# Kernel tuning notes

Hardware: AMD Instinct MI355X
Metric: run time of the kernel (lower is better)

## Reference

```python
import jax, jax.numpy as jnp
import numpy as np

INTENT_DIM = 64
HIDDEN_DIM = 128
B = 16384
M = 32


def setup_inputs() -> dict:
    key = jax.random.key(0)
    ks = jax.random.split(key, 12)
    d_in = INTENT_DIM + 4
    s = lambda n: 1.0 / np.sqrt(n)
    return {
        "ego_z": jax.random.normal(ks[0], (B, INTENT_DIM), jnp.float32),
        "neighbor_zs": jax.random.normal(ks[1], (B, M, INTENT_DIM), jnp.float32),
        "neighbor_rel_pos": jax.random.normal(ks[2], (B, M, 4), jnp.float32),
        "mask": jax.random.randint(ks[3], (B, M), 0, 2, jnp.int32),
        "Wq": jax.random.uniform(ks[4], (INTENT_DIM, HIDDEN_DIM), jnp.float32, -s(INTENT_DIM), s(INTENT_DIM)),
        "bq": jnp.zeros((HIDDEN_DIM,), jnp.float32),
        "Wk": jax.random.uniform(ks[5], (d_in, HIDDEN_DIM), jnp.float32, -s(d_in), s(d_in)),
        "bk": jnp.zeros((HIDDEN_DIM,), jnp.float32),
        "Wv": jax.random.uniform(ks[6], (d_in, HIDDEN_DIM), jnp.float32, -s(d_in), s(d_in)),
        "bv": jnp.zeros((HIDDEN_DIM,), jnp.float32),
        "Wo": jax.random.uniform(ks[7], (HIDDEN_DIM, INTENT_DIM), jnp.float32, -s(HIDDEN_DIM), s(HIDDEN_DIM)),
        "bo": jnp.zeros((INTENT_DIM,), jnp.float32),
    }


def reference(ego_z, neighbor_zs, neighbor_rel_pos, mask,
              Wq, bq, Wk, bk, Wv, bv, Wo, bo):
    # concat neighbor intent + relative position: (B, M, intent+4)
    feats = jnp.concatenate([neighbor_zs, neighbor_rel_pos], axis=-1)
    q = ego_z @ Wq + bq                       # (B, H)
    k = feats @ Wk + bk                       # (B, M, H)
    v = feats @ Wv + bv                       # (B, M, H)
    scores = jnp.einsum("bh,bmh->bm", q, k) / jnp.sqrt(jnp.float32(HIDDEN_DIM))
    scores = jnp.where(mask == 0, jnp.float32(-1e9), scores)
    weights = jax.nn.softmax(scores, axis=-1)  # (B, M)
    ctx = jnp.einsum("bm,bmh->bh", weights, v)  # (B, H)
    return ctx @ Wo + bo                        # (B, intent)
```

## Files before the change

kernel.cpp:

```cpp
#include <hip/hip_runtime.h>
#include <math.h>

#define M       32
#define IDIM    64
#define DIN     68
#define HDIM    128

#define WS_A4     0
#define WS_WVO4   4352
#define WS_U0     8704
#define WS_G      8772
#define WS_C0     8836
#define WS_OUTB   8840
#define WS_FLOATS 8904

#define CST_FLOATS 8704
#define CST_WVO    4352

template <int CTRL>
__device__ __forceinline__ float dpp_add(float x) {
  int t = __builtin_amdgcn_update_dpp(0, __float_as_int(x), CTRL, 0xF, 0xF, true);
  return x + __int_as_float(t);
}
__device__ __forceinline__ float red4(float x) {
  x = dpp_add<0xB1>(x);
  x = dpp_add<0x4E>(x);
  return x;
}
__device__ __forceinline__ float red16(float x) {
  x = dpp_add<0xB1>(x);
  x = dpp_add<0x4E>(x);
  x = dpp_add<0x124>(x);
  x = dpp_add<0x128>(x);
  return x;
}

#define SEG_A   0
#define SEG_W   17408
#define SEG_U0  34816
#define SEG_G   35088
#define SEG_OB  35344
#define SEG_C0  35600
#define PRE_T   35601

__global__ __launch_bounds__(256)
void ga_precompute(const float* __restrict__ Wq, const float* __restrict__ bq,
                   const float* __restrict__ Wk, const float* __restrict__ bk,
                   const float* __restrict__ Wv, const float* __restrict__ bv,
                   const float* __restrict__ Wo, const float* __restrict__ bo,
                   float* __restrict__ ws) {
  int t = blockIdx.x * 256 + threadIdx.x;
  if (t >= PRE_T) return;
  const float4* Wq4 = (const float4*)Wq;
  const float4* Wk4 = (const float4*)Wk;
  const float4* Wv4 = (const float4*)Wv;
  const float4* bq4 = (const float4*)bq;
  const float4* bk4 = (const float4*)bk;
  const int sub = t & 3;
  const int h4b = sub * 8;

  if (t < SEG_W) {
    int e = t >> 2;
    int k = e & 3, rem = e >> 2;
    int d = rem % DIN, i4 = rem / DIN;
    int i = i4 * 4 + k;
    float acc = 0.f;
    #pragma unroll
    for (int hh = 0; hh < 8; ++hh) {
      float4 a = Wq4[i*32 + h4b + hh], b = Wk4[d*32 + h4b + hh];
      acc = fmaf(a.x, b.x, acc); acc = fmaf(a.y, b.y, acc);
      acc = fmaf(a.z, b.z, acc); acc = fmaf(a.w, b.w, acc);
    }
    acc = red4(acc);
    if (sub == 0) ws[WS_A4 + e] = acc;
  } else if (t < SEG_U0) {
    int e = (t - SEG_W) >> 2;
    int k = e & 3, rem = e >> 2;
    int j = rem & 63, d4 = rem >> 6;
    int d = d4 * 4 + k;
    float acc = 0.f;
    #pragma unroll
    for (int hh = 0; hh < 8; ++hh) {
      float4 v = Wv4[d*32 + h4b + hh];
      int h = (h4b + hh) * 4;
      acc = fmaf(v.x, Wo[(h    )*IDIM + j], acc);
      acc = fmaf(v.y, Wo[(h + 1)*IDIM + j], acc);
      acc = fmaf(v.z, Wo[(h + 2)*IDIM + j], acc);
      acc = fmaf(v.w, Wo[(h + 3)*IDIM + j], acc);
    }
    acc = red4(acc);
    if (sub == 0) ws[WS_WVO4 + e] = acc;
  } else if (t < SEG_G) {
    int d = (t - SEG_U0) >> 2;
    float acc = 0.f;
    #pragma unroll
    for (int hh = 0; hh < 8; ++hh) {
      float4 a = Wk4[d*32 + h4b + hh], b = bq4[h4b + hh];
      acc = fmaf(a.x, b.x, acc); acc = fmaf(a.y, b.y, acc);
      acc = fmaf(a.z, b.z, acc); acc = fmaf(a.w, b.w, acc);
    }
    acc = red4(acc);
    if (sub == 0) ws[WS_U0 + d] = acc;
  } else if (t < SEG_OB) {
    int i = (t - SEG_G) >> 2;
    float acc = 0.f;
    #pragma unroll
    for (int hh = 0; hh < 8; ++hh) {
      float4 a = Wq4[i*32 + h4b + hh], b = bk4[h4b + hh];
      acc = fmaf(a.x, b.x, acc); acc = fmaf(a.y, b.y, acc);
      acc = fmaf(a.z, b.z, acc); acc = fmaf(a.w, b.w, acc);
    }
    acc = red4(acc);
    if (sub == 0) ws[WS_G + i] = acc;
  } else if (t < SEG_C0) {
    int j = (t - SEG_OB) >> 2;
    float acc = 0.f;
    #pragma unroll
    for (int hh = 0; hh < 8; ++hh) {
      int h = (h4b + hh) * 4;
      acc = fmaf(bv[h    ], Wo[(h    )*IDIM + j], acc);
      acc = fmaf(bv[h + 1], Wo[(h + 1)*IDIM + j], acc);
      acc = fmaf(bv[h + 2], Wo[(h + 2)*IDIM + j], acc);
      acc = fmaf(bv[h + 3], Wo[(h + 3)*IDIM + j], acc);
    }
    acc = red4(acc);
    if (sub == 0) ws[WS_OUTB + j] = acc + bo[j];
  } else {
    float acc = 0.f;
    for (int h = 0; h < HDIM; ++h) acc = fmaf(bq[h], bk[h], acc);
    ws[WS_C0] = acc;
  }
}

__global__ __launch_bounds__(512, 4)
void ga_main(const float* __restrict__ ego,
             const float* __restrict__ nz,
             const float* __restrict__ rp,
             const int*   __restrict__ mask,
             const float* __restrict__ ws,
             float* __restrict__ out) {
  __shared__ float cst   [CST_FLOATS];
  __shared__ float u_lds [8 * 64];
  __shared__ float fb_lds[8 * 64];

  const int tid  = threadIdx.x;
  const int wave = tid >> 6;
  const int lane = tid & 63;
  const int t4   = lane >> 4;
  const int l    = lane & 15;
  const int row  = __builtin_amdgcn_readfirstlane(blockIdx.x * 8 + wave);

  #define GLL(K) do { int c = wave + 8*(K); if (c < 34)                         \
    __builtin_amdgcn_global_load_lds(                                           \
      (const __attribute__((address_space(1))) void*)(ws + c*256 + lane*4),     \
      (__attribute__((address_space(3))) void*)(cst + c*256), 16, 0, 0); } while(0)
  GLL(0); GLL(1); GLL(2); GLL(3); GLL(4);
  #undef GLL
  __builtin_amdgcn_sched_barrier(0);

  const float4* zsrc4 = (const float4*)(nz + (size_t)row * (M * IDIM));
  float4 z0 = zsrc4[0*64 + lane], z1 = zsrc4[1*64 + lane];
  float4 z2 = zsrc4[2*64 + lane], z3 = zsrc4[3*64 + lane];
  float4 z4 = zsrc4[4*64 + lane], z5 = zsrc4[5*64 + lane];
  float4 z6 = zsrc4[6*64 + lane], z7 = zsrc4[7*64 + lane];
  const float4* rpsrc = (const float4*)(rp + (size_t)row * (M * 4));
  const float4 rpa = rpsrc[4 * (lane & 7) + t4];
  const int    mreg = mask[row * M + (lane & 31)];

  __builtin_amdgcn_sched_barrier(0);
  asm volatile("s_waitcnt vmcnt(10)" ::: "memory");
  __builtin_amdgcn_s_barrier();
  asm volatile("" ::: "memory");

  const float* egoR = ego + (size_t)row * IDIM;
  {
    float ua0 = 0.f, ua1 = 0.f, ua2 = 0.f, ua3 = 0.f;
    #pragma unroll 8
    for (int i4 = 0; i4 < 16; ++i4) {
      const float4 av = *(const float4*)&cst[(i4 * DIN + lane) << 2];
      ua0 = fmaf(egoR[i4 * 4],     av.x, ua0);
      ua1 = fmaf(egoR[i4 * 4 + 1], av.y, ua1);
      ua2 = fmaf(egoR[i4 * 4 + 2], av.z, ua2);
      ua3 = fmaf(egoR[i4 * 4 + 3], av.w, ua3);
    }
    u_lds[wave * 64 + lane] = ((ua0 + ua1) + (ua2 + ua3)) + ws[WS_U0 + lane];
  }
  float rpdot;
  {
    const float4 av = *(const float4*)&cst[(l * DIN + IDIM + t4) << 2];
    float pt = egoR[l * 4] * av.x;
    pt = fmaf(egoR[l * 4 + 1], av.y, pt);
    pt = fmaf(egoR[l * 4 + 2], av.z, pt);
    pt = fmaf(egoR[l * 4 + 3], av.w, pt);
    pt = red16(pt);
    int pti = __float_as_int(pt);
    float uh0 = __int_as_float(__builtin_amdgcn_readlane(pti, 0))  + ws[WS_U0 + 64];
    float uh1 = __int_as_float(__builtin_amdgcn_readlane(pti, 16)) + ws[WS_U0 + 65];
    float uh2 = __int_as_float(__builtin_amdgcn_readlane(pti, 32)) + ws[WS_U0 + 66];
    float uh3 = __int_as_float(__builtin_amdgcn_readlane(pti, 48)) + ws[WS_U0 + 67];
    rpdot = fmaf(rpa.w, uh3, fmaf(rpa.z, uh2, fmaf(rpa.y, uh1, rpa.x * uh0)));
  }
  float cterm;
  {
    float pc = egoR[lane] * ws[WS_G + lane];
    pc = red16(pc);
    pc += __shfl_xor(pc, 16);
    pc += __shfl_xor(pc, 32);
    cterm = pc + ws[WS_C0];
  }

  asm volatile("" ::: "memory");

  const float4 u4 = *(const float4*)&u_lds[wave * 64 + l * 4];
  const unsigned int mbits  = (unsigned int)__ballot(mreg != 0);
  const unsigned int mshift = mbits >> t4;

  #define SC(IT, Z) float s##IT; {                                        \
    float p = (Z).x * u4.x;                                               \
    p = fmaf((Z).y, u4.y, p);                                             \
    p = fmaf((Z).z, u4.z, p);                                             \
    p = fmaf((Z).w, u4.w, p);                                             \
    p += (l == (IT)) ? rpdot : 0.f;                                       \
    p = red16(p);                                                         \
    s##IT = ((mshift >> (4*(IT))) & 1u)                                   \
          ? (p + cterm) * 0.088388347648318447f : -1e9f; }
  SC(0, z0) SC(1, z1) SC(2, z2) SC(3, z3)
  SC(4, z4) SC(5, z5) SC(6, z6) SC(7, z7)
  #undef SC

  float mx = fmaxf(fmaxf(fmaxf(s0, s1), fmaxf(s2, s3)),
                   fmaxf(fmaxf(s4, s5), fmaxf(s6, s7)));
  mx = fmaxf(mx, __shfl_xor(mx, 16));
  mx = fmaxf(mx, __shfl_xor(mx, 32));
  float e0 = __expf(s0 - mx), e1 = __expf(s1 - mx);
  float e2 = __expf(s2 - mx), e3 = __expf(s3 - mx);
  float e4 = __expf(s4 - mx), e5 = __expf(s5 - mx);
  float e6 = __expf(s6 - mx), e7 = __expf(s7 - mx);
  float se = ((e0 + e1) + (e2 + e3)) + ((e4 + e5) + (e6 + e7));
  se += __shfl_xor(se, 16);
  se += __shfl_xor(se, 32);
  const float rse = __builtin_amdgcn_rcpf(se);
  const float w0 = e0 * rse, w1 = e1 * rse, w2 = e2 * rse, w3 = e3 * rse;
  const float w4 = e4 * rse, w5 = e5 * rse, w6 = e6 * rse, w7 = e7 * rse;

  float p40 = 0.f, p41 = 0.f, p42 = 0.f, p43 = 0.f;
  #define FB(W, Z) do {                                                   \
    p40 = fmaf((W), (Z).x, p40);                                          \
    p41 = fmaf((W), (Z).y, p41);                                          \
    p42 = fmaf((W), (Z).z, p42);                                          \
    p43 = fmaf((W), (Z).w, p43);                                          \
  } while (0);
  FB(w0, z0) FB(w1, z1) FB(w2, z2) FB(w3, z3)
  FB(w4, z4) FB(w5, z5) FB(w6, z6) FB(w7, z7)
  #undef FB
  p40 += __shfl_xor(p40, 16);  p40 += __shfl_xor(p40, 32);
  p41 += __shfl_xor(p41, 16);  p41 += __shfl_xor(p41, 32);
  p42 += __shfl_xor(p42, 16);  p42 += __shfl_xor(p42, 32);
  p43 += __shfl_xor(p43, 16);  p43 += __shfl_xor(p43, 32);
  if (lane < 16) {
    float4 fv; fv.x = p40; fv.y = p41; fv.z = p42; fv.w = p43;
    *(float4*)&fb_lds[wave * 64 + l * 4] = fv;
  }

  float wsel;
  {
    float a0 = (l & 1) ? w1 : w0, a1 = (l & 1) ? w3 : w2;
    float a2 = (l & 1) ? w5 : w4, a3 = (l & 1) ? w7 : w6;
    float b0 = (l & 2) ? a1 : a0, b1 = (l & 2) ? a3 : a2;
    wsel = 0.5f * ((l & 4) ? b1 : b0);
  }
  float pr0 = wsel * rpa.x, pr1 = wsel * rpa.y;
  float pr2 = wsel * rpa.z, pr3 = wsel * rpa.w;
  pr0 = red16(pr0); pr0 += __shfl_xor(pr0, 16); pr0 += __shfl_xor(pr0, 32);
  pr1 = red16(pr1); pr1 += __shfl_xor(pr1, 16); pr1 += __shfl_xor(pr1, 32);
  pr2 = red16(pr2); pr2 += __shfl_xor(pr2, 16); pr2 += __shfl_xor(pr2, 32);
  pr3 = red16(pr3); pr3 += __shfl_xor(pr3, 16); pr3 += __shfl_xor(pr3, 32);

  asm volatile("" ::: "memory");

  float oa0 = 0.f, oa1 = 0.f, oa2 = 0.f, oa3 = 0.f;
  #pragma unroll 8
  for (int d4 = 0; d4 < 16; ++d4) {
    const float4 wv = *(const float4*)&cst[CST_WVO + ((d4 * IDIM + lane) << 2)];
    const float4 fv = *(const float4*)&fb_lds[wave * 64 + d4 * 4];
    oa0 = fmaf(fv.x, wv.x, oa0);
    oa1 = fmaf(fv.y, wv.y, oa1);
    oa2 = fmaf(fv.z, wv.z, oa2);
    oa3 = fmaf(fv.w, wv.w, oa3);
  }
  {
    const float4 wv = *(const float4*)&cst[CST_WVO + ((16 * IDIM + lane) << 2)];
    oa0 = fmaf(pr0, wv.x, oa0);
    oa1 = fmaf(pr1, wv.y, oa1);
    oa2 = fmaf(pr2, wv.z, oa2);
    oa3 = fmaf(pr3, wv.w, oa3);
  }
  out[(size_t)row * IDIM + lane] = ((oa0 + oa1) + (oa2 + oa3)) + ws[WS_OUTB + lane];
}

extern "C" void kernel_launch(void* const* d_in, const int* in_sizes, int n_in,
                              void* d_out, int out_size, void* d_ws, size_t ws_size,
                              hipStream_t stream) {
  const float* ego = (const float*)d_in[0];
  const float* nz  = (const float*)d_in[1];
  const float* rp  = (const float*)d_in[2];
  const int*   mk  = (const int*)d_in[3];
  const float* Wq  = (const float*)d_in[4];
  const float* bq  = (const float*)d_in[5];
  const float* Wk  = (const float*)d_in[6];
  const float* bk  = (const float*)d_in[7];
  const float* Wv  = (const float*)d_in[8];
  const float* bv  = (const float*)d_in[9];
  const float* Wo  = (const float*)d_in[10];
  const float* bo  = (const float*)d_in[11];
  float* ws = (float*)d_ws;
  float* o  = (float*)d_out;

  const int nrows = in_sizes[0] / IDIM;

  ga_precompute<<<(PRE_T + 255) / 256, 256, 0, stream>>>(
      Wq, bq, Wk, bk, Wv, bv, Wo, bo, ws);
  ga_main<<<nrows / 8, 512, 0, stream>>>(ego, nz, rp, mk, ws, o);
}
```

Measured before the change: 38.24 us.

## Process two rows per wave with software-prefetch of next row's neighbors

Each wave now handles two batch rows instead of one, halving the grid. While the first row's softmax-weighted sum is finishing, the second row's neighbor features, relative positions and mask are loaded into registers, so the global load latency overlaps compute. The per-block constant LDS fill is also amortized over twice as many rows. The cost is higher register pressure, fewer blocks to hide latency, and a reuse of the ego-row and rpa registers that must stay consistent with the prefetch.

```diff
diff --git a/kernel.cpp b/kernel.cpp
--- a/kernel.cpp
+++ b/kernel.cpp
@@ -148,7 +148,20 @@
   const int lane = tid & 63;
   const int t4   = lane >> 4;
   const int l    = lane & 15;
-  const int row  = __builtin_amdgcn_readfirstlane(blockIdx.x * 8 + wave);
+  const int row0 = blockIdx.x * 16 + wave;
+
+  float4 z0, z1, z2, z3, z4, z5, z6, z7, rpa;
+  int mreg;
+
+  #define LOADROW(R) do {                                                      \
+    const float4* zs = (const float4*)(nz + (size_t)(R) * (M * IDIM));         \
+    z0 = zs[0*64 + lane]; z1 = zs[1*64 + lane];                                \
+    z2 = zs[2*64 + lane]; z3 = zs[3*64 + lane];                                \
+    z4 = zs[4*64 + lane]; z5 = zs[5*64 + lane];                                \
+    z6 = zs[6*64 + lane]; z7 = zs[7*64 + lane];                                \
+    rpa  = ((const float4*)(rp + (size_t)(R) * (M * 4)))[4 * (lane & 7) + t4]; \
+    mreg = mask[(R) * M + (lane & 31)];                                        \
+  } while (0)
 
   #define GLL(K) do { int c = wave + 8*(K); if (c < 34)                         \
     __builtin_amdgcn_global_load_lds(                                           \
@@ -158,144 +171,159 @@
   #undef GLL
   __builtin_amdgcn_sched_barrier(0);
 
-  const float4* zsrc4 = (const float4*)(nz + (size_t)row * (M * IDIM));
-  float4 z0 = zsrc4[0*64 + lane], z1 = zsrc4[1*64 + lane];
-  float4 z2 = zsrc4[2*64 + lane], z3 = zsrc4[3*64 + lane];
-  float4 z4 = zsrc4[4*64 + lane], z5 = zsrc4[5*64 + lane];
-  float4 z6 = zsrc4[6*64 + lane], z7 = zsrc4[7*64 + lane];
-  const float4* rpsrc = (const float4*)(rp + (size_t)row * (M * 4));
-  const float4 rpa = rpsrc[4 * (lane & 7) + t4];
-  const int    mreg = mask[row * M + (lane & 31)];
-
+  LOADROW(row0);
   __builtin_amdgcn_sched_barrier(0);
   asm volatile("s_waitcnt vmcnt(10)" ::: "memory");
   __builtin_amdgcn_s_barrier();
   asm volatile("" ::: "memory");
 
-  const float* egoR = ego + (size_t)row * IDIM;
+  #define PROCESS(R, NR) do {                                                  \
+    const int rr = __builtin_amdgcn_readfirstlane(R);                          \
+    const float* egoR = ego + (size_t)rr * IDIM;                               \
+                                                            \
+    {                                                                          \
+      float ua0 = 0.f, ua1 = 0.f, ua2 = 0.f, ua3 = 0.f;                        \
+      _Pragma("unroll 8")                                                      \
+      for (int i4 = 0; i4 < 16; ++i4) {                                        \
+        const float4 av = *(const float4*)&cst[(i4 * DIN + lane) << 2];        \
+        ua0 = fmaf(egoR[i4 * 4],     av.x, ua0);                               \
+        ua1 = fmaf(egoR[i4 * 4 + 1], av.y, ua1);                               \
+        ua2 = fmaf(egoR[i4 * 4 + 2], av.z, ua2);                               \
+        ua3 = fmaf(egoR[i4 * 4 + 3], av.w, ua3);                               \
+      }                                                                        \
+      u_lds[wave * 64 + lane] = ((ua0 + ua1) + (ua2 + ua3)) + ws[WS_U0 + lane];\
+    }                                                                          \
+    float rpdot;                                                               \
+    {                                                                          \
+      const float4 av = *(const float4*)&cst[(l * DIN + IDIM + t4) << 2];      \
+      float pt = egoR[l * 4] * av.x;                                           \
+      pt = fmaf(egoR[l * 4 + 1], av.y, pt);                                    \
+      pt = fmaf(egoR[l * 4 + 2], av.z, pt);                                    \
+      pt = fmaf(egoR[l * 4 + 3], av.w, pt);                                    \
+      pt = red16(pt);                                                          \
+      int pti = __float_as_int(pt);                                            \
+      float uh0 = __int_as_float(__builtin_amdgcn_readlane(pti, 0))            \
+                + ws[WS_U0 + 64];                                              \
+      float uh1 = __int_as_float(__builtin_amdgcn_readlane(pti, 16))           \
+                + ws[WS_U0 + 65];                                              \
+      float uh2 = __int_as_float(__builtin_amdgcn_readlane(pti, 32))           \
+                + ws[WS_U0 + 66];                                              \
+      float uh3 = __int_as_float(__builtin_amdgcn_readlane(pti, 48))           \
+                + ws[WS_U0 + 67];                                              \
+      rpdot = fmaf(rpa.w, uh3, fmaf(rpa.z, uh2, fmaf(rpa.y, uh1,               \
+              rpa.x * uh0)));                                                  \
+    }                                                                          \
+    float cterm;                                                               \
+    {                                                                          \
+      float pc = egoR[lane] * ws[WS_G + lane];                                 \
+      pc = red16(pc);                                                          \
+      pc += __shfl_xor(pc, 16);                                                \
+      pc += __shfl_xor(pc, 32);                                                \
+      cterm = pc + ws[WS_C0];                                                  \
+    }                                                                          \
+    asm volatile("" ::: "memory");                                             \
+                                                          \
+    const float4 u4 = *(const float4*)&u_lds[wave * 64 + l * 4];               \
+    const unsigned int mbits  = (unsigned int)__ballot(mreg != 0);             \
+    const unsigned int mshift = mbits >> t4;                                   \
+    float s0, s1, s2, s3, s4, s5, s6, s7;                                      \
+    SC(0, z0, s0) SC(1, z1, s1) SC(2, z2, s2) SC(3, z3, s3)                    \
+    SC(4, z4, s4) SC(5, z5, s5) SC(6, z6, s6) SC(7, z7, s7)                    \
+    float mx = fmaxf(fmaxf(fmaxf(s0, s1), fmaxf(s2, s3)),                      \
+                     fmaxf(fmaxf(s4, s5), fmaxf(s6, s7)));                     \
+    mx = fmaxf(mx, __shfl_xor(mx, 16));                                        \
+    mx = fmaxf(mx, __shfl_xor(mx, 32));                                        \
+    float e0 = __expf(s0 - mx), e1 = __expf(s1 - mx);                          \
+    float e2 = __expf(s2 - mx), e3 = __expf(s3 - mx);                          \
+    float e4 = __expf(s4 - mx), e5 = __expf(s5 - mx);                          \
+    float e6 = __expf(s6 - mx), e7 = __expf(s7 - mx);                          \
+    float se = ((e0 + e1) + (e2 + e3)) + ((e4 + e5) + (e6 + e7));              \
+    se += __shfl_xor(se, 16);                                                  \
+    se += __shfl_xor(se, 32);                                                  \
+    const float rse = __builtin_amdgcn_rcpf(se);                               \
+    const float w0 = e0 * rse, w1 = e1 * rse, w2 = e2 * rse, w3 = e3 * rse;    \
+    const float w4 = e4 * rse, w5 = e5 * rse, w6 = e6 * rse, w7 = e7 * rse;    \
+                                                            \
+    float p40 = 0.f, p41 = 0.f, p42 = 0.f, p43 = 0.f;                          \
+    FBm(w0, z0) FBm(w1, z1) FBm(w2, z2) FBm(w3, z3)                            \
+    FBm(w4, z4) FBm(w5, z5) FBm(w6, z6) FBm(w7, z7)                            \
+     \
+    if ((NR) >= 0) { LOADROW(NR); }                                            \
+    p40 += __shfl_xor(p40, 16);  p40 += __shfl_xor(p40, 32);                   \
+    p41 += __shfl_xor(p41, 16);  p41 += __shfl_xor(p41, 32);                   \
+    p42 += __shfl_xor(p42, 16);  p42 += __shfl_xor(p42, 32);                   \
+    p43 += __shfl_xor(p43, 16);  p43 += __shfl_xor(p43, 32);                   \
+    if (lane < 16) {                                                           \
+      float4 fv; fv.x = p40; fv.y = p41; fv.z = p42; fv.w = p43;               \
+      *(float4*)&fb_lds[wave * 64 + l * 4] = fv;                               \
+    }                                                                          \
+                 \
+    float wsel;                                                                \
+    {                                                                          \
+      float a0 = (l & 1) ? w1 : w0, a1 = (l & 1) ? w3 : w2;                    \
+      float a2 = (l & 1) ? w5 : w4, a3 = (l & 1) ? w7 : w6;                    \
+      float b0 = (l & 2) ? a1 : a0, b1 = (l & 2) ? a3 : a2;                    \
+      wsel = 0.5f * ((l & 4) ? b1 : b0);                                       \
+    }                                                                          \
+    float pr0 = wsel * rpold.x, pr1 = wsel * rpold.y;                          \
+    float pr2 = wsel * rpold.z, pr3 = wsel * rpold.w;                          \
+    pr0 = red16(pr0); pr0 += __shfl_xor(pr0, 16); pr0 += __shfl_xor(pr0, 32);  \
+    pr1 = red16(pr1); pr1 += __shfl_xor(pr1, 16); pr1 += __shfl_xor(pr1, 32);  \
+    pr2 = red16(pr2); pr2 += __shfl_xor(pr2, 16); pr2 += __shfl_xor(pr2, 32);  \
+    pr3 = red16(pr3); pr3 += __shfl_xor(pr3, 16); pr3 += __shfl_xor(pr3, 32);  \
+    asm volatile("" ::: "memory");                                             \
+                                                                  \
+    float oa0 = 0.f, oa1 = 0.f, oa2 = 0.f, oa3 = 0.f;                          \
+    _Pragma("unroll 8")                                                        \
+    for (int d4 = 0; d4 < 16; ++d4) {                                          \
+      const float4 wv = *(const float4*)&cst[CST_WVO + ((d4*IDIM + lane)<<2)]; \
+      const float4 fv = *(const float4*)&fb_lds[wave * 64 + d4 * 4];           \
+      oa0 = fmaf(fv.x, wv.x, oa0);                                             \
+      oa1 = fmaf(fv.y, wv.y, oa1);                                             \
+      oa2 = fmaf(fv.z, wv.z, oa2);                                             \
+      oa3 = fmaf(fv.w, wv.w, oa3);                                             \
+    }                                                                          \
+    {                                                                          \
+      const float4 wv = *(const float4*)&cst[CST_WVO + ((16*IDIM + lane)<<2)]; \
+      oa0 = fmaf(pr0, wv.x, oa0);                                              \
+      oa1 = fmaf(pr1, wv.y, oa1);                                              \
+      oa2 = fmaf(pr2, wv.z, oa2);                                              \
+      oa3 = fmaf(pr3, wv.w, oa3);                                              \
+    }                                                                          \
+    out[(size_t)rr * IDIM + lane] =                                            \
+        ((oa0 + oa1) + (oa2 + oa3)) + ws[WS_OUTB + lane];                      \
+    asm volatile("" ::: "memory");                                             \
+  } while (0)
+
+  #define SC(IT, Z, SD) {                                                      \
+    float p = (Z).x * u4.x;                                                    \
+    p = fmaf((Z).y, u4.y, p);                                                  \
+    p = fmaf((Z).z, u4.z, p);                                                  \
+    p = fmaf((Z).w, u4.w, p);                                                  \
+    p += (l == (IT)) ? rpdot : 0.f;                                            \
+    p = red16(p);                                                              \
+    SD = ((mshift >> (4*(IT))) & 1u)                                           \
+       ? (p + cterm) * 0.088388347648318447f : -1e9f; }
+  #define FBm(W, Z) do {                                                       \
+    p40 = fmaf((W), (Z).x, p40);                                               \
+    p41 = fmaf((W), (Z).y, p41);                                               \
+    p42 = fmaf((W), (Z).z, p42);                                               \
+    p43 = fmaf((W), (Z).w, p43);                                               \
+  } while (0);
+
   {
-    float ua0 = 0.f, ua1 = 0.f, ua2 = 0.f, ua3 = 0.f;
-    #pragma unroll 8
-    for (int i4 = 0; i4 < 16; ++i4) {
-      const float4 av = *(const float4*)&cst[(i4 * DIN + lane) << 2];
-      ua0 = fmaf(egoR[i4 * 4],     av.x, ua0);
-      ua1 = fmaf(egoR[i4 * 4 + 1], av.y, ua1);
-      ua2 = fmaf(egoR[i4 * 4 + 2], av.z, ua2);
-      ua3 = fmaf(egoR[i4 * 4 + 3], av.w, ua3);
-    }
-    u_lds[wave * 64 + lane] = ((ua0 + ua1) + (ua2 + ua3)) + ws[WS_U0 + lane];
-  }
-  float rpdot;
-  {
-    const float4 av = *(const float4*)&cst[(l * DIN + IDIM + t4) << 2];
-    float pt = egoR[l * 4] * av.x;
-    pt = fmaf(egoR[l * 4 + 1], av.y, pt);
-    pt = fmaf(egoR[l * 4 + 2], av.z, pt);
-    pt = fmaf(egoR[l * 4 + 3], av.w, pt);
-    pt = red16(pt);
-    int pti = __float_as_int(pt);
-    float uh0 = __int_as_float(__builtin_amdgcn_readlane(pti, 0))  + ws[WS_U0 + 64];
-    float uh1 = __int_as_float(__builtin_amdgcn_readlane(pti, 16)) + ws[WS_U0 + 65];
-    float uh2 = __int_as_float(__builtin_amdgcn_readlane(pti, 32)) + ws[WS_U0 + 66];
-    float uh3 = __int_as_float(__builtin_amdgcn_readlane(pti, 48)) + ws[WS_U0 + 67];
-    rpdot = fmaf(rpa.w, uh3, fmaf(rpa.z, uh2, fmaf(rpa.y, uh1, rpa.x * uh0)));
-  }
-  float cterm;
-  {
-    float pc = egoR[lane] * ws[WS_G + lane];
-    pc = red16(pc);
-    pc += __shfl_xor(pc, 16);
-    pc += __shfl_xor(pc, 32);
-    cterm = pc + ws[WS_C0];
-  }
-
-  asm volatile("" ::: "memory");
-
-  const float4 u4 = *(const float4*)&u_lds[wave * 64 + l * 4];
-  const unsigned int mbits  = (unsigned int)__ballot(mreg != 0);
-  const unsigned int mshift = mbits >> t4;
-
-  #define SC(IT, Z) float s##IT; {                                        \
-    float p = (Z).x * u4.x;                                               \
-    p = fmaf((Z).y, u4.y, p);                                             \
-    p = fmaf((Z).z, u4.z, p);                                             \
-    p = fmaf((Z).w, u4.w, p);                                             \
-    p += (l == (IT)) ? rpdot : 0.f;                                       \
-    p = red16(p);                                                         \
-    s##IT = ((mshift >> (4*(IT))) & 1u)                                   \
-          ? (p + cterm) * 0.088388347648318447f : -1e9f; }
-  SC(0, z0) SC(1, z1) SC(2, z2) SC(3, z3)
-  SC(4, z4) SC(5, z5) SC(6, z6) SC(7, z7)
-  #undef SC
-
-  float mx = fmaxf(fmaxf(fmaxf(s0, s1), fmaxf(s2, s3)),
-                   fmaxf(fmaxf(s4, s5), fmaxf(s6, s7)));
-  mx = fmaxf(mx, __shfl_xor(mx, 16));
-  mx = fmaxf(mx, __shfl_xor(mx, 32));
-  float e0 = __expf(s0 - mx), e1 = __expf(s1 - mx);
-  float e2 = __expf(s2 - mx), e3 = __expf(s3 - mx);
-  float e4 = __expf(s4 - mx), e5 = __expf(s5 - mx);
-  float e6 = __expf(s6 - mx), e7 = __expf(s7 - mx);
-  float se = ((e0 + e1) + (e2 + e3)) + ((e4 + e5) + (e6 + e7));
-  se += __shfl_xor(se, 16);
-  se += __shfl_xor(se, 32);
-  const float rse = __builtin_amdgcn_rcpf(se);
-  const float w0 = e0 * rse, w1 = e1 * rse, w2 = e2 * rse, w3 = e3 * rse;
-  const float w4 = e4 * rse, w5 = e5 * rse, w6 = e6 * rse, w7 = e7 * rse;
-
-  float p40 = 0.f, p41 = 0.f, p42 = 0.f, p43 = 0.f;
-  #define FB(W, Z) do {                                                   \
-    p40 = fmaf((W), (Z).x, p40);                                          \
-    p41 = fmaf((W), (Z).y, p41);                                          \
-    p42 = fmaf((W), (Z).z, p42);                                          \
-    p43 = fmaf((W), (Z).w, p43);                                          \
-  } while (0);
-  FB(w0, z0) FB(w1, z1) FB(w2, z2) FB(w3, z3)
-  FB(w4, z4) FB(w5, z5) FB(w6, z6) FB(w7, z7)
-  #undef FB
-  p40 += __shfl_xor(p40, 16);  p40 += __shfl_xor(p40, 32);
-  p41 += __shfl_xor(p41, 16);  p41 += __shfl_xor(p41, 32);
-  p42 += __shfl_xor(p42, 16);  p42 += __shfl_xor(p42, 32);
-  p43 += __shfl_xor(p43, 16);  p43 += __shfl_xor(p43, 32);
-  if (lane < 16) {
-    float4 fv; fv.x = p40; fv.y = p41; fv.z = p42; fv.w = p43;
-    *(float4*)&fb_lds[wave * 64 + l * 4] = fv;
-  }
-
-  float wsel;
-  {
-    float a0 = (l & 1) ? w1 : w0, a1 = (l & 1) ? w3 : w2;
-    float a2 = (l & 1) ? w5 : w4, a3 = (l & 1) ? w7 : w6;
-    float b0 = (l & 2) ? a1 : a0, b1 = (l & 2) ? a3 : a2;
-    wsel = 0.5f * ((l & 4) ? b1 : b0);
-  }
-  float pr0 = wsel * rpa.x, pr1 = wsel * rpa.y;
-  float pr2 = wsel * rpa.z, pr3 = wsel * rpa.w;
-  pr0 = red16(pr0); pr0 += __shfl_xor(pr0, 16); pr0 += __shfl_xor(pr0, 32);
-  pr1 = red16(pr1); pr1 += __shfl_xor(pr1, 16); pr1 += __shfl_xor(pr1, 32);
-  pr2 = red16(pr2); pr2 += __shfl_xor(pr2, 16); pr2 += __shfl_xor(pr2, 32);
-  pr3 = red16(pr3); pr3 += __shfl_xor(pr3, 16); pr3 += __shfl_xor(pr3, 32);
-
-  asm volatile("" ::: "memory");
-
-  float oa0 = 0.f, oa1 = 0.f, oa2 = 0.f, oa3 = 0.f;
-  #pragma unroll 8
-  for (int d4 = 0; d4 < 16; ++d4) {
-    const float4 wv = *(const float4*)&cst[CST_WVO + ((d4 * IDIM + lane) << 2)];
-    const float4 fv = *(const float4*)&fb_lds[wave * 64 + d4 * 4];
-    oa0 = fmaf(fv.x, wv.x, oa0);
-    oa1 = fmaf(fv.y, wv.y, oa1);
-    oa2 = fmaf(fv.z, wv.z, oa2);
-    oa3 = fmaf(fv.w, wv.w, oa3);
+    const float4 rpold = rpa;
+    PROCESS(row0, row0 + 8);
   }
   {
-    const float4 wv = *(const float4*)&cst[CST_WVO + ((16 * IDIM + lane) << 2)];
-    oa0 = fmaf(pr0, wv.x, oa0);
-    oa1 = fmaf(pr1, wv.y, oa1);
-    oa2 = fmaf(pr2, wv.z, oa2);
-    oa3 = fmaf(pr3, wv.w, oa3);
+    const float4 rpold = rpa;
+    PROCESS(row0 + 8, -1);
   }
-  out[(size_t)row * IDIM + lane] = ((oa0 + oa1) + (oa2 + oa3)) + ws[WS_OUTB + lane];
+
+  #undef PROCESS
+  #undef SC
+  #undef FBm
+  #undef LOADROW
 }
 
 extern "C" void kernel_launch(void* const* d_in, const int* in_sizes, int n_in,
@@ -320,5 +348,5 @@
 
   ga_precompute<<<(PRE_T + 255) / 256, 256, 0, stream>>>(
       Wq, bq, Wk, bk, Wv, bv, Wo, bo, ws);
-  ga_main<<<nrows / 8, 512, 0, stream>>>(ego, nz, rp, mk, ws, o);
-}
+  ga_main<<<nrows / 16, 512, 0, stream>>>(ego, nz, rp, mk, ws, o);
+}
```

After: 38.49 us. No clear change (+0.7%).

## Read fused Wv·Wo weights from global/L2 and broadcast fb via readlane

Applied to the files above, without the earlier changes.

Stops staging the second weight block (WvWo) into LDS, which halves the shared-memory footprint and the global_load_lds preamble. The final projection now reads those weights directly from global memory, where they should be L2-cached. The per-row fb vector is broadcast with v_readlane instead of a round trip through LDS. This should allow higher occupancy and shorter block startup, at the cost of global-load latency inside the output loop and sixty-four scalar readlanes.

```diff
diff --git a/kernel.cpp b/kernel.cpp
--- a/kernel.cpp
+++ b/kernel.cpp
@@ -14,8 +14,7 @@
 #define WS_OUTB   8840
 #define WS_FLOATS 8904
 
-#define CST_FLOATS 8704
-#define CST_WVO    4352
+#define CST_FLOATS 4352
 
 template <int CTRL>
 __device__ __forceinline__ float dpp_add(float x) {
@@ -33,6 +32,9 @@
   x = dpp_add<0x124>(x);
   x = dpp_add<0x128>(x);
   return x;
+}
+__device__ __forceinline__ float rdlane(float x, int sl) {
+  return __int_as_float(__builtin_amdgcn_readlane(__float_as_int(x), sl));
 }
 
 #define SEG_A   0
@@ -139,9 +141,8 @@
              const int*   __restrict__ mask,
              const float* __restrict__ ws,
              float* __restrict__ out) {
-  __shared__ float cst   [CST_FLOATS];
-  __shared__ float u_lds [8 * 64];
-  __shared__ float fb_lds[8 * 64];
+  __shared__ float cst  [CST_FLOATS];
+  __shared__ float u_lds[8 * 64];
 
   const int tid  = threadIdx.x;
   const int wave = tid >> 6;
@@ -150,11 +151,11 @@
   const int l    = lane & 15;
   const int row  = __builtin_amdgcn_readfirstlane(blockIdx.x * 8 + wave);
 
-  #define GLL(K) do { int c = wave + 8*(K); if (c < 34)                         \
+  #define GLL(K) do { int c = wave + 8*(K); if (c < 17)                         \
     __builtin_amdgcn_global_load_lds(                                           \
       (const __attribute__((address_space(1))) void*)(ws + c*256 + lane*4),     \
       (__attribute__((address_space(3))) void*)(cst + c*256), 16, 0, 0); } while(0)
-  GLL(0); GLL(1); GLL(2); GLL(3); GLL(4);
+  GLL(0); GLL(1); GLL(2);
   #undef GLL
   __builtin_amdgcn_sched_barrier(0);
 
@@ -193,11 +194,10 @@
     pt = fmaf(egoR[l * 4 + 2], av.z, pt);
     pt = fmaf(egoR[l * 4 + 3], av.w, pt);
     pt = red16(pt);
-    int pti = __float_as_int(pt);
-    float uh0 = __int_as_float(__builtin_amdgcn_readlane(pti, 0))  + ws[WS_U0 + 64];
-    float uh1 = __int_as_float(__builtin_amdgcn_readlane(pti, 16)) + ws[WS_U0 + 65];
-    float uh2 = __int_as_float(__builtin_amdgcn_readlane(pti, 32)) + ws[WS_U0 + 66];
-    float uh3 = __int_as_float(__builtin_amdgcn_readlane(pti, 48)) + ws[WS_U0 + 67];
+    float uh0 = rdlane(pt, 0)  + ws[WS_U0 + 64];
+    float uh1 = rdlane(pt, 16) + ws[WS_U0 + 65];
+    float uh2 = rdlane(pt, 32) + ws[WS_U0 + 66];
+    float uh3 = rdlane(pt, 48) + ws[WS_U0 + 67];
     rpdot = fmaf(rpa.w, uh3, fmaf(rpa.z, uh2, fmaf(rpa.y, uh1, rpa.x * uh0)));
   }
   float cterm;
@@ -257,10 +257,6 @@
   p41 += __shfl_xor(p41, 16);  p41 += __shfl_xor(p41, 32);
   p42 += __shfl_xor(p42, 16);  p42 += __shfl_xor(p42, 32);
   p43 += __shfl_xor(p43, 16);  p43 += __shfl_xor(p43, 32);
-  if (lane < 16) {
-    float4 fv; fv.x = p40; fv.y = p41; fv.z = p42; fv.w = p43;
-    *(float4*)&fb_lds[wave * 64 + l * 4] = fv;
-  }
 
   float wsel;
   {
@@ -276,20 +272,18 @@
   pr2 = red16(pr2); pr2 += __shfl_xor(pr2, 16); pr2 += __shfl_xor(pr2, 32);
   pr3 = red16(pr3); pr3 += __shfl_xor(pr3, 16); pr3 += __shfl_xor(pr3, 32);
 
-  asm volatile("" ::: "memory");
-
+  const float4* wvo4 = (const float4*)(ws + WS_WVO4);
   float oa0 = 0.f, oa1 = 0.f, oa2 = 0.f, oa3 = 0.f;
-  #pragma unroll 8
+  #pragma unroll
   for (int d4 = 0; d4 < 16; ++d4) {
-    const float4 wv = *(const float4*)&cst[CST_WVO + ((d4 * IDIM + lane) << 2)];
-    const float4 fv = *(const float4*)&fb_lds[wave * 64 + d4 * 4];
-    oa0 = fmaf(fv.x, wv.x, oa0);
-    oa1 = fmaf(fv.y, wv.y, oa1);
-    oa2 = fmaf(fv.z, wv.z, oa2);
-    oa3 = fmaf(fv.w, wv.w, oa3);
-  }
-  {
-    const float4 wv = *(const float4*)&cst[CST_WVO + ((16 * IDIM + lane) << 2)];
+    const float4 wv = wvo4[d4 * IDIM + lane];
+    oa0 = fmaf(rdlane(p40, d4), wv.x, oa0);
+    oa1 = fmaf(rdlane(p41, d4), wv.y, oa1);
+    oa2 = fmaf(rdlane(p42, d4), wv.z, oa2);
+    oa3 = fmaf(rdlane(p43, d4), wv.w, oa3);
+  }
+  {
+    const float4 wv = wvo4[16 * IDIM + lane];
     oa0 = fmaf(pr0, wv.x, oa0);
     oa1 = fmaf(pr1, wv.y, oa1);
     oa2 = fmaf(pr2, wv.z, oa2);
```

New measurement: 39.48 us. +3.3%, slower.
